# Kernel tuning notes

Measured on AMD Instinct MI355X. Metric: run time of the kernel, lower is better.

Reference implementation:

```python
import jax, jax.numpy as jnp
import numpy as np

B, F, U, A, H = 8192, 1024, 256, 16, 8  # batch, in_features, units_layer, num_actions, hidden(=8)


def _coagent_layer(x, W0, b0, W1, b1, W2, b2):
    # x: [B, f_in]; stacked weights for U independent tiny MLPs (grouped GEMMs)
    h = jax.nn.relu(jnp.einsum('bf,uhf->buh', x, W0) + b0)   # [B, U, H]
    h = jax.nn.relu(jnp.einsum('buh,ugh->bug', h, W1) + b1)  # [B, U, H]
    q = jnp.einsum('bug,uag->bua', h, W2) + b2               # [B, U, A]
    # greedy action per coagent (epsilon-greedy with greedy=True / epsilon=0)
    return jnp.argmax(q, axis=-1).astype(jnp.float32)        # [B, U]


def setup_inputs() -> dict:
    key = jax.random.key(0)
    ks = jax.random.split(key, 19)
    n = lambda k, shape, fan: (jax.random.normal(k, shape, dtype=jnp.float32)
                               / jnp.sqrt(jnp.float32(fan)))
    return {
        'state': jax.random.normal(ks[0], (B, F), dtype=jnp.float32),
        # coagent layer 0: in_features -> 8 -> 8 -> A, stacked over U units
        'W0_0': n(ks[1], (U, H, F), F), 'b0_0': jnp.zeros((U, H), jnp.float32),
        'W1_0': n(ks[2], (U, H, H), H), 'b1_0': jnp.zeros((U, H), jnp.float32),
        'W2_0': n(ks[3], (U, A, H), H), 'b2_0': jnp.zeros((U, A), jnp.float32),
        # coagent layer 1: units_layer -> 8 -> 8 -> A, stacked over U units
        'W0_1': n(ks[4], (U, H, U), U), 'b0_1': jnp.zeros((U, H), jnp.float32),
        'W1_1': n(ks[5], (U, H, H), H), 'b1_1': jnp.zeros((U, H), jnp.float32),
        'W2_1': n(ks[6], (U, A, H), H), 'b2_1': jnp.zeros((U, A), jnp.float32),
        # Policy head: units_layer -> 8 -> 8 -> 1
        'PW0': n(ks[7], (H, U), U), 'Pb0': jnp.zeros((H,), jnp.float32),
        'PW1': n(ks[8], (H, H), H), 'Pb1': jnp.zeros((H,), jnp.float32),
        'PW2': n(ks[9], (1, H), H), 'Pb2': jnp.zeros((1,), jnp.float32),
    }


def reference(state, W0_0, b0_0, W1_0, b1_0, W2_0, b2_0,
              W0_1, b0_1, W1_1, b1_1, W2_1, b2_1,
              PW0, Pb0, PW1, Pb1, PW2, Pb2):
    a0 = _coagent_layer(state, W0_0, b0_0, W1_0, b1_0, W2_0, b2_0)  # [B, U]
    a1 = _coagent_layer(a0, W0_1, b0_1, W1_1, b1_1, W2_1, b2_1)     # [B, U]
    h = jax.nn.relu(a1 @ PW0.T + Pb0)
    h = jax.nn.relu(h @ PW1.T + Pb1)
    return h @ PW2.T + Pb2  # [B, 1]
```

## Files before the change

kernel.cpp:

```cpp
#include <hip/hip_runtime.h>
#include <cstring>
#include <cstdint>

#define B_TOTAL 8192
#define F_IN    1024
#define U_UNITS 256
#define NACT    16
#define HID     8

typedef float    f32x4  __attribute__((ext_vector_type(4)));
typedef _Float16 half8  __attribute__((ext_vector_type(8)));
typedef _Float16 half4  __attribute__((ext_vector_type(4)));


__global__ __launch_bounds__(256)
void pack3_kernel(const float* __restrict__ s0, _Float16* __restrict__ d0h, _Float16* __restrict__ d0l,
                  const float* __restrict__ s1, _Float16* __restrict__ d1h, _Float16* __restrict__ d1l,
                  const float* __restrict__ s2, _Float16* __restrict__ d2h, _Float16* __restrict__ d2l)
{
    constexpr int NB0 = (B_TOTAL / 16) * (F_IN / 128);
    constexpr int NB1 = (U_UNITS * HID / 16) * (F_IN / 128);
    __shared__ float ls[16 * 132];
    int b = blockIdx.x;
    const float* src; _Float16 *dh, *dl; int K, lg;
    if (b < NB0)            { src = s0; dh = d0h; dl = d0l; K = F_IN;    lg = 3; }
    else if (b < NB0 + NB1) { b -= NB0; src = s1; dh = d1h; dl = d1l; K = F_IN; lg = 3; }
    else                    { b -= NB0 + NB1; src = s2; dh = d2h; dl = d2l; K = U_UNITS; lg = 1; }

    const int tid = threadIdx.x;
    const int mt  = b >> lg;
    const int kb  = b & ((1 << lg) - 1);
    const int r0  = mt * 16;

#pragma unroll
    for (int i = 0; i < 2; ++i) {
        const int e = tid + (i << 8);
        const int row = e >> 5;
        const int c4  = e & 31;
        f32x4 v = *reinterpret_cast<const f32x4*>(
            &src[(size_t)(r0 + row) * K + (kb << 7) + (c4 << 2)]);
        *reinterpret_cast<f32x4*>(&ls[row * 132 + (c4 << 2)]) = v;
    }
    __syncthreads();

    const int k8 = tid >> 4, r = tid & 15;
    float x[8];
#pragma unroll
    for (int j = 0; j < 8; ++j) x[j] = ls[r * 132 + (k8 << 3) + j];
    half8 h, l;
#pragma unroll
    for (int j = 0; j < 8; ++j) {
        h[j] = (_Float16)x[j];
        l[j] = (_Float16)((x[j] - (float)h[j]) * 2048.0f);
    }
    const size_t off = (((size_t)mt * (K >> 5)) + (kb << 2) + (k8 >> 2)) * 512
                     + (size_t)(((k8 & 3) << 4) + r) * 8;
    *reinterpret_cast<half8*>(&dh[off]) = h;
    *reinterpret_cast<half8*>(&dl[off]) = l;
}

constexpr int BM = 128, BN = 128;

template<int K_TOTAL, bool A_SPLIT, bool OUT_TF32>
__global__ __launch_bounds__(256, 2)
void coagent_mfma(const _Float16* __restrict__ Ahg, const _Float16* __restrict__ Alg,
                  const _Float16* __restrict__ Bhg, const _Float16* __restrict__ Blg,
                  const float* __restrict__ b0, const float* __restrict__ W1,
                  const float* __restrict__ b1, const float* __restrict__ W2,
                  const float* __restrict__ b2, void* __restrict__ outp)
{
    struct EpiBufs { float Hs[BM][65]; _Float16 ab[BM * 8]; };
    __shared__ EpiBufs sm;

    constexpr int NTK = K_TOTAL >> 5;
    constexpr size_t TS = (size_t)NTK * 512;

    const int tid  = threadIdx.x;
    const int wave = tid >> 6;
    const int lane = tid & 63;
    const int quad = lane >> 4;
    const int l15  = lane & 15;
    const int wm   = (wave >> 1) * 64;
    const int m0   = blockIdx.y * BM;
    const int n0   = blockIdx.x * BN;

    const int at = (wave >> 1) * 4;
    const int bt = (wave & 1) * 4;

    const _Float16* Ah0 = Ahg + ((size_t)((m0 >> 4) + at)) * TS + lane * 8;
    const _Float16* Al0 = A_SPLIT ? (Alg + ((size_t)((m0 >> 4) + at)) * TS + lane * 8) : nullptr;
    const _Float16* Bh0 = Bhg + ((size_t)((n0 >> 4) + bt)) * TS + lane * 8;
    const _Float16* Bl0 = Blg + ((size_t)((n0 >> 4) + bt)) * TS + lane * 8;

    f32x4 acc1[4][4];
    f32x4 acc2[4][4];
#pragma unroll
    for (int i = 0; i < 4; ++i)
#pragma unroll
        for (int j = 0; j < 4; ++j) { acc1[i][j] = {0.f,0.f,0.f,0.f}; acc2[i][j] = {0.f,0.f,0.f,0.f}; }

    for (int kt = 0; kt < NTK; ++kt) {
        const size_t ko = (size_t)kt * 512;
        half8 af[4], bf[4], xa[4], xb[4];
#pragma unroll
        for (int mt = 0; mt < 4; ++mt)
            af[mt] = *reinterpret_cast<const half8*>(Ah0 + mt * TS + ko);
#pragma unroll
        for (int nt = 0; nt < 4; ++nt)
            bf[nt] = *reinterpret_cast<const half8*>(Bh0 + nt * TS + ko);
        if (A_SPLIT) {
#pragma unroll
            for (int mt = 0; mt < 4; ++mt)
                xa[mt] = *reinterpret_cast<const half8*>(Al0 + mt * TS + ko);
        }
#pragma unroll
        for (int nt = 0; nt < 4; ++nt)
            xb[nt] = *reinterpret_cast<const half8*>(Bl0 + nt * TS + ko);

#pragma unroll
        for (int mt = 0; mt < 4; ++mt)
#pragma unroll
            for (int nt = 0; nt < 4; ++nt)
                acc1[mt][nt] = __builtin_amdgcn_mfma_f32_16x16x32_f16(af[mt], bf[nt], acc1[mt][nt], 0, 0, 0);
        if (A_SPLIT) {
#pragma unroll
            for (int mt = 0; mt < 4; ++mt)
#pragma unroll
                for (int nt = 0; nt < 4; ++nt)
                    acc2[mt][nt] = __builtin_amdgcn_mfma_f32_16x16x32_f16(xa[mt], bf[nt], acc2[mt][nt], 0, 0, 0);
        }
#pragma unroll
        for (int mt = 0; mt < 4; ++mt)
#pragma unroll
            for (int nt = 0; nt < 4; ++nt)
                acc2[mt][nt] = __builtin_amdgcn_mfma_f32_16x16x32_f16(af[mt], xb[nt], acc2[mt][nt], 0, 0, 0);
    }

    const int ubase = n0 >> 3;
    for (int half = 0; half < 2; ++half) {
        __syncthreads();
        if ((wave & 1) == half) {
#pragma unroll
            for (int mt = 0; mt < 4; ++mt)
#pragma unroll
                for (int nt = 0; nt < 4; ++nt)
#pragma unroll
                    for (int r = 0; r < 4; ++r)
                        sm.Hs[wm + mt * 16 + quad * 4 + r][nt * 16 + l15] =
                            acc1[mt][nt][r] + acc2[mt][nt][r] * (1.0f / 2048.0f);
        }
        __syncthreads();
#pragma unroll
        for (int p = 0; p < 4; ++p) {
            const int pair = (p << 8) + tid;
            const int ul = pair >> 7;
            const int bl = pair & 127;
            const int u  = __builtin_amdgcn_readfirstlane(ubase + half * 8 + ul);
            const float* __restrict__ b0u = b0 + u * 8;
            const float* __restrict__ W1u = W1 + u * 64;
            const float* __restrict__ b1u = b1 + u * 8;
            const float* __restrict__ W2u = W2 + u * 128;
            const float* __restrict__ b2u = b2 + u * 16;

            float h[HID];
#pragma unroll
            for (int j = 0; j < HID; ++j)
                h[j] = fmaxf(sm.Hs[bl][ul * 8 + j] + b0u[j], 0.f);

            float h2[HID];
#pragma unroll
            for (int g = 0; g < HID; ++g) {
                float s = b1u[g];
#pragma unroll
                for (int j = 0; j < HID; ++j)
                    s += h[j] * W1u[g * 8 + j];
                h2[g] = fmaxf(s, 0.f);
            }

            float best = b2u[0];
#pragma unroll
            for (int j = 0; j < HID; ++j) best += h2[j] * W2u[j];
            int bi = 0;
#pragma unroll
            for (int a = 1; a < NACT; ++a) {
                float s = b2u[a];
#pragma unroll
                for (int j = 0; j < HID; ++j)
                    s += h2[j] * W2u[a * 8 + j];
                if (s > best) { best = s; bi = a; }
            }

            if (OUT_TF32) {
                ((float*)outp)[(size_t)u * B_TOTAL + m0 + bl] = (float)bi;
            } else {
                sm.ab[bl * 8 + ul] = (_Float16)bi;
            }
        }
        if (!OUT_TF32) {
            __syncthreads();
            if (tid < 128) {
                float4 v = *reinterpret_cast<float4*>(&sm.ab[tid * 8]);
                const int u = ubase + half * 8;
                const int b = m0 + tid;
                const size_t off = ((size_t)(b >> 4) * 8 + (u >> 5)) * 512
                                 + (size_t)((((u >> 3) & 3) << 4) + (b & 15)) * 8;
                *reinterpret_cast<float4*>(&((_Float16*)outp)[off]) = v;
            }
        }
    }
}


constexpr int FBM = 128, FBN = 128, FBK = 16;

template<int K_TOTAL, bool X_TRANSPOSED>
__global__ __launch_bounds__(256, 2)
void coagent_kernel(const float* __restrict__ X, const float* __restrict__ W0,
                    const float* __restrict__ b0, const float* __restrict__ W1,
                    const float* __restrict__ b1, const float* __restrict__ W2,
                    const float* __restrict__ b2, float* __restrict__ outT)
{
    struct SMemGemm { float As[FBK][FBM + 4]; float Bs[FBK][FBN + 4]; };
    union SMem { SMemGemm g; float Hs[FBM][65]; };
    __shared__ SMem sm;

    const int tid = threadIdx.x;
    const int tx = tid & 15, ty = tid >> 4;
    const int m0 = blockIdx.y * FBM, n0 = blockIdx.x * FBN;

    float acc[8][8];
#pragma unroll
    for (int i = 0; i < 8; ++i)
#pragma unroll
        for (int j = 0; j < 8; ++j) acc[i][j] = 0.f;

    for (int k0 = 0; k0 < K_TOTAL; k0 += FBK) {
        __syncthreads();
        if (X_TRANSPOSED) {
#pragma unroll
            for (int l = tid; l < (FBM * FBK) / 4; l += 256) {
                const int k = l >> 5, q = l & 31;
                const float4 v = *reinterpret_cast<const float4*>(
                    &X[(size_t)(k0 + k) * B_TOTAL + m0 + 4 * q]);
                *reinterpret_cast<float4*>(&sm.g.As[k][4 * q]) = v;
            }
        } else {
#pragma unroll
            for (int l = tid; l < (FBM * FBK) / 4; l += 256) {
                const int row = l >> 2, c = l & 3;
                const float4 v = *reinterpret_cast<const float4*>(
                    &X[(size_t)(m0 + row) * K_TOTAL + k0 + 4 * c]);
                sm.g.As[4 * c + 0][row] = v.x; sm.g.As[4 * c + 1][row] = v.y;
                sm.g.As[4 * c + 2][row] = v.z; sm.g.As[4 * c + 3][row] = v.w;
            }
        }
#pragma unroll
        for (int l = tid; l < (FBN * FBK) / 4; l += 256) {
            const int row = l >> 2, c = l & 3;
            const float4 v = *reinterpret_cast<const float4*>(
                &W0[(size_t)(n0 + row) * K_TOTAL + k0 + 4 * c]);
            sm.g.Bs[4 * c + 0][row] = v.x; sm.g.Bs[4 * c + 1][row] = v.y;
            sm.g.Bs[4 * c + 2][row] = v.z; sm.g.Bs[4 * c + 3][row] = v.w;
        }
        __syncthreads();
#pragma unroll
        for (int k = 0; k < FBK; ++k) {
            float a[8], bb[8];
            *reinterpret_cast<float4*>(&a[0])  = *reinterpret_cast<float4*>(&sm.g.As[k][4 * ty]);
            *reinterpret_cast<float4*>(&a[4])  = *reinterpret_cast<float4*>(&sm.g.As[k][64 + 4 * ty]);
            *reinterpret_cast<float4*>(&bb[0]) = *reinterpret_cast<float4*>(&sm.g.Bs[k][4 * tx]);
            *reinterpret_cast<float4*>(&bb[4]) = *reinterpret_cast<float4*>(&sm.g.Bs[k][64 + 4 * tx]);
#pragma unroll
            for (int i = 0; i < 8; ++i)
#pragma unroll
                for (int j = 0; j < 8; ++j) acc[i][j] += a[i] * bb[j];
        }
    }

    const int ub_base = n0 >> 3;
    for (int half = 0; half < 2; ++half) {
        __syncthreads();
#pragma unroll
        for (int i = 0; i < 8; ++i) {
            const int row = (i < 4) ? (4 * ty + i) : (64 + 4 * ty + (i - 4));
#pragma unroll
            for (int j = 0; j < 4; ++j)
                sm.Hs[row][4 * tx + j] = acc[i][4 * half + j];
        }
        __syncthreads();
#pragma unroll
        for (int p = 0; p < 4; ++p) {
            const int pair = (p << 8) + tid;
            const int ul = pair >> 7, bl = pair & 127;
            const int u = ub_base + half * 8 + ul;
            float h[HID];
#pragma unroll
            for (int j = 0; j < HID; ++j)
                h[j] = fmaxf(sm.Hs[bl][ul * 8 + j] + b0[u * 8 + j], 0.f);
            float h2[HID];
#pragma unroll
            for (int g = 0; g < HID; ++g) {
                float s = b1[u * 8 + g];
#pragma unroll
                for (int j = 0; j < HID; ++j) s += h[j] * W1[u * 64 + g * 8 + j];
                h2[g] = fmaxf(s, 0.f);
            }
            float best = b2[u * 16];
#pragma unroll
            for (int j = 0; j < HID; ++j) best += h2[j] * W2[u * 128 + j];
            int bi = 0;
#pragma unroll
            for (int a = 1; a < NACT; ++a) {
                float s = b2[u * 16 + a];
#pragma unroll
                for (int j = 0; j < HID; ++j) s += h2[j] * W2[u * 128 + a * 8 + j];
                if (s > best) { best = s; bi = a; }
            }
            outT[(size_t)u * B_TOTAL + m0 + bl] = (float)bi;
        }
    }
}

__global__ __launch_bounds__(256)
void policy_kernel(const float* __restrict__ A1T,
                   const float* __restrict__ PW0, const float* __restrict__ Pb0,
                   const float* __restrict__ PW1, const float* __restrict__ Pb1,
                   const float* __restrict__ PW2, const float* __restrict__ Pb2,
                   float* __restrict__ out)
{
    __shared__ float part[8][32][HID + 1];
    const int tid = threadIdx.x;
    const int b32 = tid & 31;
    const int sl  = tid >> 5;
    const int b   = blockIdx.x * 32 + b32;

    float hp[HID];
#pragma unroll
    for (int j = 0; j < HID; ++j) hp[j] = 0.f;

#pragma unroll 1
    for (int q0 = 0; q0 < 32; q0 += 8) {
        float v[8];
#pragma unroll
        for (int t = 0; t < 8; ++t)
            v[t] = A1T[(size_t)(sl * 32 + q0 + t) * B_TOTAL + b];
#pragma unroll
        for (int t = 0; t < 8; ++t)
#pragma unroll
            for (int j = 0; j < HID; ++j)
                hp[j] += v[t] * PW0[j * U_UNITS + sl * 32 + q0 + t];
    }
#pragma unroll
    for (int j = 0; j < HID; ++j) part[sl][b32][j] = hp[j];
    __syncthreads();

    if (sl == 0) {
        float h[HID];
#pragma unroll
        for (int j = 0; j < HID; ++j) {
            float s = Pb0[j];
#pragma unroll
            for (int s8 = 0; s8 < 8; ++s8) s += part[s8][b32][j];
            h[j] = fmaxf(s, 0.f);
        }
        float h2[HID];
#pragma unroll
        for (int g = 0; g < HID; ++g) {
            float s = Pb1[g];
#pragma unroll
            for (int j = 0; j < HID; ++j) s += h[j] * PW1[g * 8 + j];
            h2[g] = fmaxf(s, 0.f);
        }
        float o = Pb2[0];
#pragma unroll
        for (int j = 0; j < HID; ++j) o += h2[j] * PW2[j];
        out[b] = o;
    }
}


extern "C" void kernel_launch(void* const* d_in, const int* in_sizes, int n_in,
                              void* d_out, int out_size, void* d_ws, size_t ws_size,
                              hipStream_t stream)
{
    const float* state = (const float*)d_in[0];
    const float* W0_0  = (const float*)d_in[1];
    const float* b0_0  = (const float*)d_in[2];
    const float* W1_0  = (const float*)d_in[3];
    const float* b1_0  = (const float*)d_in[4];
    const float* W2_0  = (const float*)d_in[5];
    const float* b2_0  = (const float*)d_in[6];
    const float* W0_1  = (const float*)d_in[7];
    const float* b0_1  = (const float*)d_in[8];
    const float* W1_1  = (const float*)d_in[9];
    const float* b1_1  = (const float*)d_in[10];
    const float* W2_1  = (const float*)d_in[11];
    const float* b2_1  = (const float*)d_in[12];
    const float* PW0   = (const float*)d_in[13];
    const float* Pb0   = (const float*)d_in[14];
    const float* PW1   = (const float*)d_in[15];
    const float* Pb1   = (const float*)d_in[16];
    const float* PW2   = (const float*)d_in[17];
    const float* Pb2   = (const float*)d_in[18];

    const size_t SZ_STATE = (size_t)B_TOTAL * F_IN;
    const size_t SZ_W00   = (size_t)U_UNITS * HID * F_IN;
    const size_t SZ_W01   = (size_t)U_UNITS * HID * U_UNITS;
    const size_t NEED = (2 * SZ_STATE + 2 * SZ_W00 + 2 * SZ_W01
                         + (size_t)B_TOTAL * U_UNITS) * 2
                        + (size_t)U_UNITS * B_TOTAL * 4;

    if (ws_size >= NEED) {
        char* p = (char*)d_ws;
        _Float16* state_h = (_Float16*)p;                p += SZ_STATE * 2;
        _Float16* state_l = (_Float16*)p;                p += SZ_STATE * 2;
        _Float16* w00_h   = (_Float16*)p;                p += SZ_W00 * 2;
        _Float16* w00_l   = (_Float16*)p;                p += SZ_W00 * 2;
        _Float16* w01_h   = (_Float16*)p;                p += SZ_W01 * 2;
        _Float16* w01_l   = (_Float16*)p;                p += SZ_W01 * 2;
        _Float16* a0      = (_Float16*)p;                p += (size_t)B_TOTAL * U_UNITS * 2;
        float*    a1T     = (float*)p;

        constexpr int NB0 = (B_TOTAL / 16) * (F_IN / 128);
        constexpr int NB1 = (U_UNITS * HID / 16) * (F_IN / 128);
        constexpr int NB2 = (U_UNITS * HID / 16) * (U_UNITS / 128);
        pack3_kernel<<<NB0 + NB1 + NB2, 256, 0, stream>>>(
            state, state_h, state_l, W0_0, w00_h, w00_l, W0_1, w01_h, w01_l);

        dim3 grid((U_UNITS * HID) / BN, B_TOTAL / BM);

        coagent_mfma<F_IN, true, false><<<grid, 256, 0, stream>>>(
            state_h, state_l, w00_h, w00_l, b0_0, W1_0, b1_0, W2_0, b2_0, (void*)a0);

        coagent_mfma<U_UNITS, false, true><<<grid, 256, 0, stream>>>(
            a0, nullptr, w01_h, w01_l, b0_1, W1_1, b1_1, W2_1, b2_1, (void*)a1T);

        policy_kernel<<<B_TOTAL / 32, 256, 0, stream>>>(
            a1T, PW0, Pb0, PW1, Pb1, PW2, Pb2, (float*)d_out);
    } else {
        float* a0T = (float*)d_ws;
        float* a1T = a0T + (size_t)U_UNITS * B_TOTAL;
        dim3 grid((U_UNITS * HID) / FBN, B_TOTAL / FBM);
        coagent_kernel<F_IN, false><<<grid, 256, 0, stream>>>(
            state, W0_0, b0_0, W1_0, b1_0, W2_0, b2_0, a0T);
        coagent_kernel<U_UNITS, true><<<grid, 256, 0, stream>>>(
            a0T, W0_1, b0_1, W1_1, b1_1, W2_1, b2_1, a1T);
        policy_kernel<<<B_TOTAL / 32, 256, 0, stream>>>(
            a1T, PW0, Pb0, PW1, Pb1, PW2, Pb2, (float*)d_out);
    }
}
```

Before: 320.8 us.

## Stage layer-0 MFMA operands through double-buffered LDS with prefetch

For the first coagent GEMM, each K-step's A/B hi/lo fragments are now loaded cooperatively into a double-buffered shared-memory stage, with the next tile's global loads issued before the MFMAs and written to the other buffer afterwards. This removes duplicate global loads across waves, since each wave pair previously fetched the same fragments independently, and overlaps memory latency with compute. The epilogue also drops readfirstlane on the unit index and indexes the weights directly. The staging buffer (64KB) shares a union with the epilogue buffers, which raises LDS use and may limit two-blocks-per-CU occupancy.

```diff
diff --git a/kernel.cpp b/kernel.cpp
--- a/kernel.cpp
+++ b/kernel.cpp
@@ -1,6 +1,7 @@
 #include <hip/hip_runtime.h>
 #include <cstring>
 #include <cstdint>
+#include <type_traits>
 
 #define B_TOTAL 8192
 #define F_IN    1024
@@ -61,7 +62,11 @@
 
 constexpr int BM = 128, BN = 128;
 
-template<int K_TOTAL, bool A_SPLIT, bool OUT_TF32>
+struct EpiBufs { float Hs[BM][65]; _Float16 ab[BM * 8]; };
+struct SMemStaged { union { _Float16 stage[2][16384]; EpiBufs e; }; };
+struct SMemPlain  { EpiBufs e; };
+
+template<int K_TOTAL, bool A_SPLIT, bool OUT_TF32, bool STAGED>
 __global__ __launch_bounds__(256, 2)
 void coagent_mfma(const _Float16* __restrict__ Ahg, const _Float16* __restrict__ Alg,
                   const _Float16* __restrict__ Bhg, const _Float16* __restrict__ Blg,
@@ -69,8 +74,8 @@
                   const float* __restrict__ b1, const float* __restrict__ W2,
                   const float* __restrict__ b2, void* __restrict__ outp)
 {
-    struct EpiBufs { float Hs[BM][65]; _Float16 ab[BM * 8]; };
-    __shared__ EpiBufs sm;
+    using SMem = typename std::conditional<STAGED, SMemStaged, SMemPlain>::type;
+    __shared__ SMem sm;
 
     constexpr int NTK = K_TOTAL >> 5;
     constexpr size_t TS = (size_t)NTK * 512;
@@ -87,11 +92,6 @@
     const int at = (wave >> 1) * 4;
     const int bt = (wave & 1) * 4;
 
-    const _Float16* Ah0 = Ahg + ((size_t)((m0 >> 4) + at)) * TS + lane * 8;
-    const _Float16* Al0 = A_SPLIT ? (Alg + ((size_t)((m0 >> 4) + at)) * TS + lane * 8) : nullptr;
-    const _Float16* Bh0 = Bhg + ((size_t)((n0 >> 4) + bt)) * TS + lane * 8;
-    const _Float16* Bl0 = Blg + ((size_t)((n0 >> 4) + bt)) * TS + lane * 8;
-
     f32x4 acc1[4][4];
     f32x4 acc2[4][4];
 #pragma unroll
@@ -99,41 +99,120 @@
 #pragma unroll
         for (int j = 0; j < 4; ++j) { acc1[i][j] = {0.f,0.f,0.f,0.f}; acc2[i][j] = {0.f,0.f,0.f,0.f}; }
 
-    for (int kt = 0; kt < NTK; ++kt) {
-        const size_t ko = (size_t)kt * 512;
-        half8 af[4], bf[4], xa[4], xb[4];
-#pragma unroll
-        for (int mt = 0; mt < 4; ++mt)
-            af[mt] = *reinterpret_cast<const half8*>(Ah0 + mt * TS + ko);
-#pragma unroll
-        for (int nt = 0; nt < 4; ++nt)
-            bf[nt] = *reinterpret_cast<const half8*>(Bh0 + nt * TS + ko);
-        if (A_SPLIT) {
-#pragma unroll
-            for (int mt = 0; mt < 4; ++mt)
-                xa[mt] = *reinterpret_cast<const half8*>(Al0 + mt * TS + ko);
-        }
-#pragma unroll
-        for (int nt = 0; nt < 4; ++nt)
-            xb[nt] = *reinterpret_cast<const half8*>(Bl0 + nt * TS + ko);
-
-#pragma unroll
-        for (int mt = 0; mt < 4; ++mt)
+    if constexpr (STAGED) {
+        const _Float16* gs[8];
+        uint32_t lo[8];
+#pragma unroll
+        for (int j = 0; j < 8; ++j) {
+            const int c = j * 256 + tid;
+            const int p = c >> 9;
+            const int t = (c >> 6) & 7;
+            const int l = c & 63;
+            const _Float16* base = (p == 0) ? Ahg : (p == 1) ? Alg
+                                 : (p == 2) ? Bhg : Blg;
+            const int rt = (((p <= 1) ? m0 : n0) >> 4) + t;
+            gs[j] = base + (size_t)rt * TS + (uint32_t)l * 8;
+            lo[j] = (uint32_t)c * 8;
+        }
+        {
+            half8 st[8];
+#pragma unroll
+            for (int j = 0; j < 8; ++j) st[j] = *reinterpret_cast<const half8*>(gs[j]);
+#pragma unroll
+            for (int j = 0; j < 8; ++j)
+                *reinterpret_cast<half8*>(&sm.stage[0][lo[j]]) = st[j];
+        }
+
+        for (int kt = 0; kt < NTK; ++kt) {
+            __syncthreads();
+            const int par = kt & 1;
+            const _Float16* sb = &sm.stage[par][0];
+
+            half8 af[4], bf[4], xa[4], xb[4], st[8];
+#pragma unroll
+            for (int mt = 0; mt < 4; ++mt)
+                af[mt] = *reinterpret_cast<const half8*>(&sb[(size_t)((at + mt) * 64 + lane) * 8]);
 #pragma unroll
             for (int nt = 0; nt < 4; ++nt)
-                acc1[mt][nt] = __builtin_amdgcn_mfma_f32_16x16x32_f16(af[mt], bf[nt], acc1[mt][nt], 0, 0, 0);
-        if (A_SPLIT) {
+                bf[nt] = *reinterpret_cast<const half8*>(&sb[(size_t)((16 + bt + nt) * 64 + lane) * 8]);
+#pragma unroll
+            for (int mt = 0; mt < 4; ++mt)
+                xa[mt] = *reinterpret_cast<const half8*>(&sb[(size_t)((8 + at + mt) * 64 + lane) * 8]);
+
+            const bool more = (kt + 1 < NTK);
+            if (more) {
+#pragma unroll
+                for (int j = 0; j < 8; ++j)
+                    st[j] = *reinterpret_cast<const half8*>(gs[j] + (size_t)(kt + 1) * 512);
+            }
+
+#pragma unroll
+            for (int mt = 0; mt < 4; ++mt)
+#pragma unroll
+                for (int nt = 0; nt < 4; ++nt)
+                    acc1[mt][nt] = __builtin_amdgcn_mfma_f32_16x16x32_f16(af[mt], bf[nt], acc1[mt][nt], 0, 0, 0);
 #pragma unroll
             for (int mt = 0; mt < 4; ++mt)
 #pragma unroll
                 for (int nt = 0; nt < 4; ++nt)
                     acc2[mt][nt] = __builtin_amdgcn_mfma_f32_16x16x32_f16(xa[mt], bf[nt], acc2[mt][nt], 0, 0, 0);
-        }
-#pragma unroll
-        for (int mt = 0; mt < 4; ++mt)
 #pragma unroll
             for (int nt = 0; nt < 4; ++nt)
-                acc2[mt][nt] = __builtin_amdgcn_mfma_f32_16x16x32_f16(af[mt], xb[nt], acc2[mt][nt], 0, 0, 0);
+                xb[nt] = *reinterpret_cast<const half8*>(&sb[(size_t)((24 + bt + nt) * 64 + lane) * 8]);
+#pragma unroll
+            for (int mt = 0; mt < 4; ++mt)
+#pragma unroll
+                for (int nt = 0; nt < 4; ++nt)
+                    acc2[mt][nt] = __builtin_amdgcn_mfma_f32_16x16x32_f16(af[mt], xb[nt], acc2[mt][nt], 0, 0, 0);
+
+            if (more) {
+#pragma unroll
+                for (int j = 0; j < 8; ++j)
+                    *reinterpret_cast<half8*>(&sm.stage[1 - par][lo[j]]) = st[j];
+            }
+        }
+    } else {
+        const _Float16* Ah0 = Ahg + ((size_t)((m0 >> 4) + at)) * TS + lane * 8;
+        const _Float16* Al0 = A_SPLIT ? (Alg + ((size_t)((m0 >> 4) + at)) * TS + lane * 8) : nullptr;
+        const _Float16* Bh0 = Bhg + ((size_t)((n0 >> 4) + bt)) * TS + lane * 8;
+        const _Float16* Bl0 = Blg + ((size_t)((n0 >> 4) + bt)) * TS + lane * 8;
+
+        for (int kt = 0; kt < NTK; ++kt) {
+            const size_t ko = (size_t)kt * 512;
+            half8 af[4], bf[4], xa[4], xb[4];
+#pragma unroll
+            for (int mt = 0; mt < 4; ++mt)
+                af[mt] = *reinterpret_cast<const half8*>(Ah0 + mt * TS + ko);
+#pragma unroll
+            for (int nt = 0; nt < 4; ++nt)
+                bf[nt] = *reinterpret_cast<const half8*>(Bh0 + nt * TS + ko);
+            if (A_SPLIT) {
+#pragma unroll
+                for (int mt = 0; mt < 4; ++mt)
+                    xa[mt] = *reinterpret_cast<const half8*>(Al0 + mt * TS + ko);
+            }
+#pragma unroll
+            for (int nt = 0; nt < 4; ++nt)
+                xb[nt] = *reinterpret_cast<const half8*>(Bl0 + nt * TS + ko);
+
+#pragma unroll
+            for (int mt = 0; mt < 4; ++mt)
+#pragma unroll
+                for (int nt = 0; nt < 4; ++nt)
+                    acc1[mt][nt] = __builtin_amdgcn_mfma_f32_16x16x32_f16(af[mt], bf[nt], acc1[mt][nt], 0, 0, 0);
+            if (A_SPLIT) {
+#pragma unroll
+                for (int mt = 0; mt < 4; ++mt)
+#pragma unroll
+                    for (int nt = 0; nt < 4; ++nt)
+                        acc2[mt][nt] = __builtin_amdgcn_mfma_f32_16x16x32_f16(xa[mt], bf[nt], acc2[mt][nt], 0, 0, 0);
+            }
+#pragma unroll
+            for (int mt = 0; mt < 4; ++mt)
+#pragma unroll
+                for (int nt = 0; nt < 4; ++nt)
+                    acc2[mt][nt] = __builtin_amdgcn_mfma_f32_16x16x32_f16(af[mt], xb[nt], acc2[mt][nt], 0, 0, 0);
+        }
     }
 
     const int ubase = n0 >> 3;
@@ -146,7 +225,7 @@
                 for (int nt = 0; nt < 4; ++nt)
 #pragma unroll
                     for (int r = 0; r < 4; ++r)
-                        sm.Hs[wm + mt * 16 + quad * 4 + r][nt * 16 + l15] =
+                        sm.e.Hs[wm + mt * 16 + quad * 4 + r][nt * 16 + l15] =
                             acc1[mt][nt][r] + acc2[mt][nt][r] * (1.0f / 2048.0f);
         }
         __syncthreads();
@@ -155,51 +234,46 @@
             const int pair = (p << 8) + tid;
             const int ul = pair >> 7;
             const int bl = pair & 127;
-            const int u  = __builtin_amdgcn_readfirstlane(ubase + half * 8 + ul);
-            const float* __restrict__ b0u = b0 + u * 8;
-            const float* __restrict__ W1u = W1 + u * 64;
-            const float* __restrict__ b1u = b1 + u * 8;
-            const float* __restrict__ W2u = W2 + u * 128;
-            const float* __restrict__ b2u = b2 + u * 16;
+            const int u  = ubase + half * 8 + ul;
 
             float h[HID];
 #pragma unroll
             for (int j = 0; j < HID; ++j)
-                h[j] = fmaxf(sm.Hs[bl][ul * 8 + j] + b0u[j], 0.f);
+                h[j] = fmaxf(sm.e.Hs[bl][ul * 8 + j] + b0[u * 8 + j], 0.f);
 
             float h2[HID];
 #pragma unroll
             for (int g = 0; g < HID; ++g) {
-                float s = b1u[g];
+                float s = b1[u * 8 + g];
 #pragma unroll
                 for (int j = 0; j < HID; ++j)
-                    s += h[j] * W1u[g * 8 + j];
+                    s += h[j] * W1[u * 64 + g * 8 + j];
                 h2[g] = fmaxf(s, 0.f);
             }
 
-            float best = b2u[0];
-#pragma unroll
-            for (int j = 0; j < HID; ++j) best += h2[j] * W2u[j];
+            float best = b2[u * 16];
+#pragma unroll
+            for (int j = 0; j < HID; ++j) best += h2[j] * W2[u * 128 + j];
             int bi = 0;
 #pragma unroll
             for (int a = 1; a < NACT; ++a) {
-                float s = b2u[a];
+                float s = b2[u * 16 + a];
 #pragma unroll
                 for (int j = 0; j < HID; ++j)
-                    s += h2[j] * W2u[a * 8 + j];
+                    s += h2[j] * W2[u * 128 + a * 8 + j];
                 if (s > best) { best = s; bi = a; }
             }
 
             if (OUT_TF32) {
                 ((float*)outp)[(size_t)u * B_TOTAL + m0 + bl] = (float)bi;
             } else {
-                sm.ab[bl * 8 + ul] = (_Float16)bi;
+                sm.e.ab[bl * 8 + ul] = (_Float16)bi;
             }
         }
         if (!OUT_TF32) {
             __syncthreads();
             if (tid < 128) {
-                float4 v = *reinterpret_cast<float4*>(&sm.ab[tid * 8]);
+                float4 v = *reinterpret_cast<float4*>(&sm.e.ab[tid * 8]);
                 const int u = ubase + half * 8;
                 const int b = m0 + tid;
                 const size_t off = ((size_t)(b >> 4) * 8 + (u >> 5)) * 512
@@ -429,10 +503,10 @@
 
         dim3 grid((U_UNITS * HID) / BN, B_TOTAL / BM);
 
-        coagent_mfma<F_IN, true, false><<<grid, 256, 0, stream>>>(
+        coagent_mfma<F_IN, true, false, true><<<grid, 256, 0, stream>>>(
             state_h, state_l, w00_h, w00_l, b0_0, W1_0, b1_0, W2_0, b2_0, (void*)a0);
 
-        coagent_mfma<U_UNITS, false, true><<<grid, 256, 0, stream>>>(
+        coagent_mfma<U_UNITS, false, true, false><<<grid, 256, 0, stream>>>(
             a0, nullptr, w01_h, w01_l, b0_1, W1_1, b1_1, W2_1, b2_1, (void*)a1T);
 
         policy_kernel<<<B_TOTAL / 32, 256, 0, stream>>>(
```

Result: slower. 342.0 us (+6.6%).
